# Optimization experiments

Hardware: AMD Instinct MI355X
Metric: run time of the kernel (lower is better)

Reference implementation:

```python
import jax, jax.numpy as jnp
from jax import lax
import numpy as np

B, A, C, H, W = 256, 64, 8, 15, 15
E = 128
CONV_CH = [8, 16, 32, 16, 32]   # in -> hidden[16,32,16] -> out(32)
FLAT = 32 * 7 * 7               # four 3x3 VALID convs: 15 -> 7
MLP_DIMS = [FLAT, 128, 128, 128]


def setup_inputs() -> dict:
    key = jax.random.key(0)
    ks = jax.random.split(key, 16)
    inp = {}
    inp["states"] = jax.random.normal(ks[0], (B, A, C, H, W), jnp.float32)
    # nonnegative weighted adjacency (dense graph, diagonal included like the
    # original loop which always appends (i,i) with weight adj[b,i,i])
    inp["adjacencies"] = jax.random.uniform(ks[1], (B, A, A), jnp.float32)
    for l, (ci, co) in enumerate(zip(CONV_CH[:-1], CONV_CH[1:])):
        inp[f"cw{l}"] = jax.random.normal(ks[2 + l], (co, ci, 3, 3), jnp.float32) * 0.05
        inp[f"cb{l}"] = jnp.zeros((co,), jnp.float32)
    for l, (di, do) in enumerate(zip(MLP_DIMS[:-1], MLP_DIMS[1:])):
        inp[f"mw{l}"] = jax.random.normal(ks[8 + l], (di, do), jnp.float32) * 0.02
        inp[f"mb{l}"] = jnp.zeros((do,), jnp.float32)
    inp["gw"] = jax.random.normal(ks[12], (E, E), jnp.float32) * 0.05
    inp["gb"] = jnp.zeros((E,), jnp.float32)
    return inp


def _conv(x, w, b):
    y = lax.conv_general_dilated(x, w, (1, 1), "VALID",
                                 dimension_numbers=("NCHW", "OIHW", "NCHW"))
    return jax.nn.relu(y + b[None, :, None, None])


def reference(states, adjacencies, cw0, cb0, cw1, cb1, cw2, cb2, cw3, cb3,
              mw0, mb0, mw1, mb1, mw2, mb2, gw, gb):
    b, a, c, h, w = states.shape
    x = states.reshape(b * a, c, h, w)
    # CNN encoder (batched over all B*A agent observations at once)
    for cw, cb in ((cw0, cb0), (cw1, cb1), (cw2, cb2), (cw3, cb3)):
        x = _conv(x, cw, cb)
    x = x.reshape(b * a, -1)
    # MLP: relu on hidden layers, linear output
    x = jax.nn.relu(x @ mw0 + mb0)
    x = jax.nn.relu(x @ mw1 + mb1)
    feats = x @ mw2 + mb2                      # [B*A, E]
    feats = feats.reshape(b, a, E)
    # GCNConv(add_self_loops=False): out = D^{-1/2} A D^{-1/2} aggregation
    # edge (i,j): row=source i, col=target j; deg from target (column sums)
    xw = jnp.einsum("bae,ef->baf", feats, gw)  # x @ W
    deg = adjacencies.sum(axis=1)              # deg[b,j] = sum_i A[b,i,j]
    dinv = jnp.where(deg > 0, 1.0 / jnp.sqrt(jnp.where(deg > 0, deg, 1.0)), 0.0)
    norm = dinv[:, :, None] * adjacencies * dinv[:, None, :]  # N[b,i,j]
    out = jnp.einsum("bij,bie->bje", norm, xw) + gb            # out[b,j] = sum_i N_ij xW_i
    return out.reshape(b * a, E)
```

## Files before the change

### kernel.cpp

```cpp
#include <hip/hip_runtime.h>


typedef short short8 __attribute__((ext_vector_type(8)));
typedef float f32x4  __attribute__((ext_vector_type(4)));

__device__ __forceinline__ unsigned short f2bf(float f) {
    unsigned u = __builtin_bit_cast(unsigned, f);
    u = (u + 0x7FFFu + ((u >> 16) & 1u)) >> 16;
    return (unsigned short)u;
}
__device__ __forceinline__ float bf2f(unsigned short h) {
    unsigned u = ((unsigned)h) << 16;
    return __builtin_bit_cast(float, u);
}

#define ZED_OFF 26304
#define ARENA_FLOATS 6592

__global__ __launch_bounds__(256) void wprep(
    const float* __restrict__ cw0, const float* __restrict__ cw1,
    const float* __restrict__ cw2, const float* __restrict__ cw3,
    short* __restrict__ wbuf)
{
    int gidx = blockIdx.x * 256 + threadIdx.x;
    if (gidx >= 36864) return;
    const float* cw; int base, CI, NM, KIND;
    if (gidx < 3072)       { cw = cw0; base = 0;     CI = 8;  NM = 1; KIND = 0; }
    else if (gidx < 15360) { cw = cw1; base = 3072;  CI = 16; NM = 2; KIND = 1; }
    else if (gidx < 24576) { cw = cw2; base = 15360; CI = 32; NM = 1; KIND = 2; }
    else                   { cw = cw3; base = 24576; CI = 16; NM = 2; KIND = 1; }
    int e = gidx - base;
    int j = e & 7, lane = (e >> 3) & 63, rest = e >> 9;
    int comp = rest & 1, cm = rest >> 1;
    int m = cm % NM, c = cm / NM;
    int g = lane >> 4, colr = lane & 15;
    int co = m * 16 + colr;
    int ky, kx, ci; bool pad = false;
    if (KIND == 0)      { ky = c; kx = g; ci = j; pad = (g >= 3); }
    else if (KIND == 1) {
        ky = c >> 1; int half = c & 1;
        if (half == 0) { kx = g >> 1; ci = (g & 1) * 8 + j; }
        else           { kx = 2;      ci = (g & 1) * 8 + j; pad = (g >= 2); }
    } else              { ky = c / 3; kx = c % 3; ci = g * 8 + j; }
    float w = pad ? 0.0f : cw[((co * CI + ci) * 3 + ky) * 3 + kx];
    unsigned short h = f2bf(w);
    wbuf[gidx] = (comp == 0) ? (short)h : (short)f2bf(w - bf2f(h));
}

__global__ __launch_bounds__(256) void wprep_mlp(
    const float* __restrict__ mw0, const float* __restrict__ mw1,
    const float* __restrict__ mw2, const float* __restrict__ gw,
    short* __restrict__ wp)
{
    int gidx = blockIdx.x * 256 + threadIdx.x;
    if (gidx >= 499712) return;
    const float* W; int base;
    if (gidx < 401408)      { W = mw0; base = 0; }
    else if (gidx < 434176) { W = mw1; base = 401408; }
    else if (gidx < 466944) { W = mw2; base = 434176; }
    else                    { W = gw;  base = 466944; }
    int e = gidx - base;
    int j = e & 7, lane = (e >> 3) & 63, rest = e >> 9;
    int comp = rest & 1, knn = rest >> 1;
    int nn = knn & 7, kc = knn >> 3;
    int k = kc * 32 + (lane >> 4) * 8 + j;
    int n = nn * 16 + (lane & 15);
    float w = W[(size_t)k * 128 + n];
    unsigned short h = f2bf(w);
    wp[gidx] = (comp == 0) ? (short)h : (short)f2bf(w - bf2f(h));
}

template<int CI, int CO, int WIN, int WOUT, int POUT, int NM, int NT,
         int KIND, int INOFF, int NPIN, int OUTOFF, int GOUT>
__device__ __forceinline__ void mfma_layer(
    float* __restrict__ A, const short* __restrict__ wbuf,
    const float* __restrict__ bias, short* __restrict__ gH,
    short* __restrict__ gL, int tid)
{
    const char* Ac = (const char*)A;
    char* Aw = (char*)A;
    const int wv = tid >> 6, lane = tid & 63;
    const int g = lane >> 4, col = lane & 15;
    constexpr int UNITS = NT * NM;
    constexpr int CPK = (KIND == 0) ? 1 : (KIND == 1) ? 2 : 3;
    constexpr int DIN = (CI / 8) * NPIN * 16;
    constexpr int DOUT = (CO / 8) * POUT * 16;
    const int u0 = (UNITS * wv) >> 2, u1 = (UNITS * (wv + 1)) >> 2;

#pragma unroll 1
    for (int u = u0; u < u1; ++u) {
        const int n = u / NM, m = u - n * NM;
        const int p = n * 16 + col;
        const bool valid = (p < POUT);
        const int pix = valid ? p : (POUT - 1);
        const int y = pix / WOUT;
        const int x = pix - y * WOUT;

        f32x4 acc;
        {
            const float4 bv = *(const float4*)(bias + m * 16 + g * 4);
            acc[0] = bv.x; acc[1] = bv.y; acc[2] = bv.z; acc[3] = bv.w;
        }

#pragma unroll
        for (int ky = 0; ky < 3; ++ky) {
#pragma unroll
            for (int cc = 0; cc < CPK; ++cc) {
                int kg, kx; bool okv;
                if (KIND == 0)      { kx = g;      kg = 0;     okv = (g < 3); }
                else if (KIND == 1) {
                    if (cc == 0)    { kx = g >> 1; kg = g & 1; okv = true; }
                    else            { kx = 2;      kg = g & 1; okv = (g < 2); }
                } else              { kx = cc;     kg = g;     okv = true; }
                const int pin = (y + ky) * WIN + x + kx;
                const int vH = okv ? (INOFF + (kg * NPIN + pin) * 16) : ZED_OFF;
                const int vL = okv ? (vH + DIN) : ZED_OFF;
                const int c = ky * CPK + cc;

                const short8 Ah = *(const short8*)(
                    wbuf + ((c * NM + m) * 2 + 0) * 512 + lane * 8);
                const short8 Al = *(const short8*)(
                    wbuf + ((c * NM + m) * 2 + 1) * 512 + lane * 8);

                const short8 Bh = *(const short8*)(Ac + vH);
                acc = __builtin_amdgcn_mfma_f32_16x16x32_bf16(Ah, Bh, acc, 0, 0, 0);
                acc = __builtin_amdgcn_mfma_f32_16x16x32_bf16(Al, Bh, acc, 0, 0, 0);
                const short8 Bl = *(const short8*)(Ac + vL);
                acc = __builtin_amdgcn_mfma_f32_16x16x32_bf16(Ah, Bl, acc, 0, 0, 0);
            }
        }

        if (GOUT) {
            if (valid) {
                const int co0 = m * 16 + g * 4;
#pragma unroll
                for (int r = 0; r < 4; ++r) {
                    float v = fmaxf(acc[r], 0.0f);
                    unsigned short h = f2bf(v);
                    gH[(co0 + r) * POUT + pix] = (short)h;
                    gL[(co0 + r) * POUT + pix] = (short)f2bf(v - bf2f(h));
                }
            }
        } else if (valid) {
            unsigned hh[2], ll[2];
#pragma unroll
            for (int r2 = 0; r2 < 2; ++r2) {
                float v0 = fmaxf(acc[r2 * 2 + 0], 0.0f);
                float v1 = fmaxf(acc[r2 * 2 + 1], 0.0f);
                unsigned short h0 = f2bf(v0), h1 = f2bf(v1);
                unsigned short l0 = f2bf(v0 - bf2f(h0));
                unsigned short l1 = f2bf(v1 - bf2f(h1));
                hh[r2] = (unsigned)h0 | ((unsigned)h1 << 16);
                ll[r2] = (unsigned)l0 | ((unsigned)l1 << 16);
            }
            const int kgO = m * 2 + (g >> 1);
            const int ob2 = OUTOFF + (kgO * POUT + pix) * 16 + (g & 1) * 8;
            *(uint2*)(Aw + ob2)        = make_uint2(hh[0], hh[1]);
            *(uint2*)(Aw + ob2 + DOUT) = make_uint2(ll[0], ll[1]);
        }
    }
}

__global__ __launch_bounds__(256) void conv_mfma(
    const float* __restrict__ states, const short* __restrict__ wbuf,
    const float* __restrict__ cb0, const float* __restrict__ cb1,
    const float* __restrict__ cb2, const float* __restrict__ cb3,
    short* __restrict__ x0h, short* __restrict__ x0l)
{
    __shared__ float A[ARENA_FLOATS];
    const int tid = threadIdx.x;

    if (tid < 4) A[ZED_OFF / 4 + tid] = 0.0f;

    const float* gin = states + (size_t)blockIdx.x * 1800;
    {
        char* Aw = (char*)A;
#pragma unroll
        for (int it = 0; it < 8; ++it) {
            int e = tid + it * 256;
            if (e < 1800) {
                float f = gin[e];
                int ci = e / 225, p = e - ci * 225;
                unsigned short h = f2bf(f);
                unsigned short l = f2bf(f - bf2f(h));
                int off = 10816 + p * 16 + ci * 2;
                *(short*)(Aw + off) = (short)h;
                *(short*)(Aw + off + 3600) = (short)l;
            }
        }
    }
    __syncthreads();

    mfma_layer<8, 16, 15, 13, 169, 1, 11, 0, 10816, 225, 0, 0>(
        A, wbuf + 0, cb0, nullptr, nullptr, tid);
    __syncthreads();
    mfma_layer<16, 32, 13, 11, 121, 2, 8, 1, 0, 169, 10816, 0>(
        A, wbuf + 3072, cb1, nullptr, nullptr, tid);
    __syncthreads();
    mfma_layer<32, 16, 11, 9, 81, 1, 6, 2, 10816, 121, 0, 0>(
        A, wbuf + 15360, cb2, nullptr, nullptr, tid);
    __syncthreads();
    mfma_layer<16, 32, 9, 7, 49, 2, 4, 1, 0, 81, 0, 1>(
        A, wbuf + 24576, cb3,
        x0h + (size_t)blockIdx.x * 1568, x0l + (size_t)blockIdx.x * 1568, tid);
}

template<int KCH, bool RELU, bool OUTF32>
__global__ __launch_bounds__(256) void mgemm(
    const short* __restrict__ Ah, const short* __restrict__ Al,
    const short* __restrict__ wp, const float* __restrict__ bias,
    short* __restrict__ Ch, short* __restrict__ Cl, float* __restrict__ Cf)
{
    constexpr int K = KCH * 32;
    const int tid = threadIdx.x;
    const int wv = tid >> 6, lane = tid & 63;
    const int col = lane & 15, g = lane >> 4;
    const int row0 = blockIdx.x * 64 + wv * 16;
    const size_t aoff = (size_t)(row0 + col) * K + g * 8;

    f32x4 acc[8];
#pragma unroll
    for (int nn = 0; nn < 8; ++nn) {
        float b = bias ? bias[nn * 16 + col] : 0.0f;
        acc[nn][0] = b; acc[nn][1] = b; acc[nn][2] = b; acc[nn][3] = b;
    }

#pragma unroll 2
    for (int kc = 0; kc < KCH; ++kc) {
        const short8 fAh = *(const short8*)(Ah + aoff + kc * 32);
        const short8 fAl = *(const short8*)(Al + aoff + kc * 32);
        const short* wk = wp + (size_t)kc * 8192 + lane * 8;
#pragma unroll
        for (int nn = 0; nn < 8; ++nn) {
            const short8 Bh = *(const short8*)(wk + (nn * 2 + 0) * 512);
            const short8 Bl = *(const short8*)(wk + (nn * 2 + 1) * 512);
            acc[nn] = __builtin_amdgcn_mfma_f32_16x16x32_bf16(fAh, Bh, acc[nn], 0, 0, 0);
            acc[nn] = __builtin_amdgcn_mfma_f32_16x16x32_bf16(fAl, Bh, acc[nn], 0, 0, 0);
            acc[nn] = __builtin_amdgcn_mfma_f32_16x16x32_bf16(fAh, Bl, acc[nn], 0, 0, 0);
        }
    }

#pragma unroll
    for (int nn = 0; nn < 8; ++nn) {
#pragma unroll
        for (int r = 0; r < 4; ++r) {
            float v = acc[nn][r];
            if (RELU) v = fmaxf(v, 0.0f);
            const size_t idx = (size_t)(row0 + g * 4 + r) * 128 + nn * 16 + col;
            if (OUTF32) {
                Cf[idx] = v;
            } else {
                unsigned short h = f2bf(v);
                Ch[idx] = (short)h;
                Cl[idx] = (short)f2bf(v - bf2f(h));
            }
        }
    }
}

__global__ __launch_bounds__(256) void gcn_agg(
    const float* __restrict__ adj, const float* __restrict__ xw,
    const float* __restrict__ gb, float* __restrict__ outp)
{
    __shared__ float sAdj[64 * 64];
    __shared__ float sXW[64 * 128];
    __shared__ float sDinv[64];

    const int b = blockIdx.x;
    const int tid = threadIdx.x;

    const float* ga = adj + (size_t)b * 4096;
#pragma unroll
    for (int it = 0; it < 4; it++) {
        int idx = tid + it * 256;
        *(float4*)(sAdj + idx * 4) = *(const float4*)(ga + idx * 4);
    }
    const float* gx = xw + (size_t)b * 8192;
#pragma unroll
    for (int it = 0; it < 8; it++) {
        int idx = tid + it * 256;
        *(float4*)(sXW + idx * 4) = *(const float4*)(gx + idx * 4);
    }
    __syncthreads();

    if (tid < 64) {
        float d = 0.0f;
        for (int i = 0; i < 64; i++) d += sAdj[i * 64 + tid];
        sDinv[tid] = (d > 0.0f) ? rsqrtf(d) : 0.0f;
    }
    __syncthreads();

#pragma unroll
    for (int it = 0; it < 8; it++) {
        int idx = tid + it * 256;
        int i = idx >> 5;
        float s = sDinv[i];
        float4 v = *(float4*)(sXW + idx * 4);
        v.x *= s; v.y *= s; v.z *= s; v.w *= s;
        *(float4*)(sXW + idx * 4) = v;
    }
    __syncthreads();

    const int j  = tid >> 2;
    const int eb = (tid & 3) * 32;
    float acc[32];
#pragma unroll
    for (int e = 0; e < 32; e++) acc[e] = 0.0f;

    for (int i = 0; i < 64; i++) {
        float wgt = sAdj[i * 64 + j];
        const float* xp = sXW + i * 128 + eb;
#pragma unroll
        for (int e4 = 0; e4 < 8; e4++) {
            float4 v = *(const float4*)(xp + e4 * 4);
            acc[e4 * 4 + 0] += wgt * v.x;
            acc[e4 * 4 + 1] += wgt * v.y;
            acc[e4 * 4 + 2] += wgt * v.z;
            acc[e4 * 4 + 3] += wgt * v.w;
        }
    }

    const float dj = sDinv[j];
    float* go = outp + ((size_t)b * 64 + j) * 128 + eb;
#pragma unroll
    for (int e4 = 0; e4 < 8; e4++) {
        float4 v;
        v.x = acc[e4 * 4 + 0] * dj + gb[eb + e4 * 4 + 0];
        v.y = acc[e4 * 4 + 1] * dj + gb[eb + e4 * 4 + 1];
        v.z = acc[e4 * 4 + 2] * dj + gb[eb + e4 * 4 + 2];
        v.w = acc[e4 * 4 + 3] * dj + gb[eb + e4 * 4 + 3];
        *(float4*)(go + e4 * 4) = v;
    }
}

extern "C" void kernel_launch(void* const* d_in, const int* in_sizes, int n_in,
                              void* d_out, int out_size, void* d_ws, size_t ws_size,
                              hipStream_t stream)
{
    const float* states = (const float*)d_in[0];
    const float* adj    = (const float*)d_in[1];
    const float* cw0 = (const float*)d_in[2];  const float* cb0 = (const float*)d_in[3];
    const float* cw1 = (const float*)d_in[4];  const float* cb1 = (const float*)d_in[5];
    const float* cw2 = (const float*)d_in[6];  const float* cb2 = (const float*)d_in[7];
    const float* cw3 = (const float*)d_in[8];  const float* cb3 = (const float*)d_in[9];
    const float* mw0 = (const float*)d_in[10]; const float* mb0 = (const float*)d_in[11];
    const float* mw1 = (const float*)d_in[12]; const float* mb1 = (const float*)d_in[13];
    const float* mw2 = (const float*)d_in[14]; const float* mb2 = (const float*)d_in[15];
    const float* gw  = (const float*)d_in[16]; const float* gb  = (const float*)d_in[17];

    float* ws = (float*)d_ws;
    const size_t X0E = (size_t)16384 * 1568;

    short* X0h = (short*)ws;
    short* X0l = X0h + X0E;
    short* H1h = (short*)(ws + X0E);
    short* H1l = H1h + 2097152;
    short* H2h = (short*)(ws + X0E + 2097152);
    short* H2l = H2h + 2097152;
    short* WBc = (short*)(ws + X0E + 2 * 2097152);
    short* WPm = WBc + 36864;
    short* Fh = (short*)ws;
    short* Fl = Fh + 2097152;
    float* xw = ws + 2097152;

    float* out = (float*)d_out;

    wprep<<<144, 256, 0, stream>>>(cw0, cw1, cw2, cw3, WBc);
    wprep_mlp<<<1952, 256, 0, stream>>>(mw0, mw1, mw2, gw, WPm);
    conv_mfma<<<16384, 256, 0, stream>>>(states, WBc, cb0, cb1, cb2, cb3,
                                         X0h, X0l);
    mgemm<49, true,  false><<<256, 256, 0, stream>>>(X0h, X0l, WPm + 0,
                                                     mb0, H1h, H1l, nullptr);
    mgemm<4,  true,  false><<<256, 256, 0, stream>>>(H1h, H1l, WPm + 401408,
                                                     mb1, H2h, H2l, nullptr);
    mgemm<4,  false, false><<<256, 256, 0, stream>>>(H2h, H2l, WPm + 434176,
                                                     mb2, Fh, Fl, nullptr);
    mgemm<4,  false, true ><<<256, 256, 0, stream>>>(Fh, Fl, WPm + 466944,
                                                     nullptr, nullptr, nullptr, xw);
    gcn_agg<<<256, 256, 0, stream>>>(adj, xw, gb, out);
}
```

Before: 676.2 us.

## Fuse MLP layers and GCN aggregation into one kernel, merge weight prep kernels

Replaces the four separate MLP/GCN-weight GEMM kernels and the GCN aggregation kernel with a single per-batch kernel that keeps intermediate activations in shared memory as split bf16 hi/lo pairs. The first layer stages X0 tiles through LDS in 128-wide K chunks. The two weight-prep kernels are merged into one launch. This removes global round-trips for the hidden activations and several launch overheads, at the cost of a large LDS footprint per block and extra barriers in the long first-layer K loop.

After: 563.6 us. -16.7%, faster.

```diff
diff --git a/kernel.cpp b/kernel.cpp
--- a/kernel.cpp
+++ b/kernel.cpp
@@ -17,57 +17,54 @@
 #define ZED_OFF 26304
 #define ARENA_FLOATS 6592
 
-__global__ __launch_bounds__(256) void wprep(
+__global__ __launch_bounds__(256) void wprep_all(
     const float* __restrict__ cw0, const float* __restrict__ cw1,
     const float* __restrict__ cw2, const float* __restrict__ cw3,
-    short* __restrict__ wbuf)
+    const float* __restrict__ mw0, const float* __restrict__ mw1,
+    const float* __restrict__ mw2, const float* __restrict__ gw,
+    short* __restrict__ wbuf, short* __restrict__ wp)
 {
     int gidx = blockIdx.x * 256 + threadIdx.x;
-    if (gidx >= 36864) return;
-    const float* cw; int base, CI, NM, KIND;
-    if (gidx < 3072)       { cw = cw0; base = 0;     CI = 8;  NM = 1; KIND = 0; }
-    else if (gidx < 15360) { cw = cw1; base = 3072;  CI = 16; NM = 2; KIND = 1; }
-    else if (gidx < 24576) { cw = cw2; base = 15360; CI = 32; NM = 1; KIND = 2; }
-    else                   { cw = cw3; base = 24576; CI = 16; NM = 2; KIND = 1; }
-    int e = gidx - base;
-    int j = e & 7, lane = (e >> 3) & 63, rest = e >> 9;
-    int comp = rest & 1, cm = rest >> 1;
-    int m = cm % NM, c = cm / NM;
-    int g = lane >> 4, colr = lane & 15;
-    int co = m * 16 + colr;
-    int ky, kx, ci; bool pad = false;
-    if (KIND == 0)      { ky = c; kx = g; ci = j; pad = (g >= 3); }
-    else if (KIND == 1) {
-        ky = c >> 1; int half = c & 1;
-        if (half == 0) { kx = g >> 1; ci = (g & 1) * 8 + j; }
-        else           { kx = 2;      ci = (g & 1) * 8 + j; pad = (g >= 2); }
-    } else              { ky = c / 3; kx = c % 3; ci = g * 8 + j; }
-    float w = pad ? 0.0f : cw[((co * CI + ci) * 3 + ky) * 3 + kx];
-    unsigned short h = f2bf(w);
-    wbuf[gidx] = (comp == 0) ? (short)h : (short)f2bf(w - bf2f(h));
-}
-
-__global__ __launch_bounds__(256) void wprep_mlp(
-    const float* __restrict__ mw0, const float* __restrict__ mw1,
-    const float* __restrict__ mw2, const float* __restrict__ gw,
-    short* __restrict__ wp)
-{
-    int gidx = blockIdx.x * 256 + threadIdx.x;
-    if (gidx >= 499712) return;
-    const float* W; int base;
-    if (gidx < 401408)      { W = mw0; base = 0; }
-    else if (gidx < 434176) { W = mw1; base = 401408; }
-    else if (gidx < 466944) { W = mw2; base = 434176; }
-    else                    { W = gw;  base = 466944; }
-    int e = gidx - base;
-    int j = e & 7, lane = (e >> 3) & 63, rest = e >> 9;
-    int comp = rest & 1, knn = rest >> 1;
-    int nn = knn & 7, kc = knn >> 3;
-    int k = kc * 32 + (lane >> 4) * 8 + j;
-    int n = nn * 16 + (lane & 15);
-    float w = W[(size_t)k * 128 + n];
-    unsigned short h = f2bf(w);
-    wp[gidx] = (comp == 0) ? (short)h : (short)f2bf(w - bf2f(h));
+    if (gidx < 36864) {
+        const float* cw; int base, CI, NM, KIND;
+        if (gidx < 3072)       { cw = cw0; base = 0;     CI = 8;  NM = 1; KIND = 0; }
+        else if (gidx < 15360) { cw = cw1; base = 3072;  CI = 16; NM = 2; KIND = 1; }
+        else if (gidx < 24576) { cw = cw2; base = 15360; CI = 32; NM = 1; KIND = 2; }
+        else                   { cw = cw3; base = 24576; CI = 16; NM = 2; KIND = 1; }
+        int e = gidx - base;
+        int j = e & 7, lane = (e >> 3) & 63, rest = e >> 9;
+        int comp = rest & 1, cm = rest >> 1;
+        int m = cm % NM, c = cm / NM;
+        int g = lane >> 4, colr = lane & 15;
+        int co = m * 16 + colr;
+        int ky, kx, ci; bool pad = false;
+        if (KIND == 0)      { ky = c; kx = g; ci = j; pad = (g >= 3); }
+        else if (KIND == 1) {
+            ky = c >> 1; int half = c & 1;
+            if (half == 0) { kx = g >> 1; ci = (g & 1) * 8 + j; }
+            else           { kx = 2;      ci = (g & 1) * 8 + j; pad = (g >= 2); }
+        } else              { ky = c / 3; kx = c % 3; ci = g * 8 + j; }
+        float w = pad ? 0.0f : cw[((co * CI + ci) * 3 + ky) * 3 + kx];
+        unsigned short h = f2bf(w);
+        wbuf[gidx] = (comp == 0) ? (short)h : (short)f2bf(w - bf2f(h));
+    } else {
+        int e0 = gidx - 36864;
+        if (e0 >= 499712) return;
+        const float* W; int base;
+        if (e0 < 401408)      { W = mw0; base = 0; }
+        else if (e0 < 434176) { W = mw1; base = 401408; }
+        else if (e0 < 466944) { W = mw2; base = 434176; }
+        else                  { W = gw;  base = 466944; }
+        int e = e0 - base;
+        int j = e & 7, lane = (e >> 3) & 63, rest = e >> 9;
+        int comp = rest & 1, knn = rest >> 1;
+        int nn = knn & 7, kc = knn >> 3;
+        int k = kc * 32 + (lane >> 4) * 8 + j;
+        int n = nn * 16 + (lane & 15);
+        float w = W[(size_t)k * 128 + n];
+        unsigned short h = f2bf(w);
+        wp[e0] = (comp == 0) ? (short)h : (short)f2bf(w - bf2f(h));
+    }
 }
 
 template<int CI, int CO, int WIN, int WOUT, int POUT, int NM, int NT,
@@ -205,31 +202,82 @@
         x0h + (size_t)blockIdx.x * 1568, x0l + (size_t)blockIdx.x * 1568, tid);
 }
 
-template<int KCH, bool RELU, bool OUTF32>
-__global__ __launch_bounds__(256) void mgemm(
-    const short* __restrict__ Ah, const short* __restrict__ Al,
-    const short* __restrict__ wp, const float* __restrict__ bias,
-    short* __restrict__ Ch, short* __restrict__ Cl, float* __restrict__ Cf)
+__global__ __launch_bounds__(256) void mlp_gcn(
+    const short* __restrict__ X0h, const short* __restrict__ X0l,
+    const short* __restrict__ wp,
+    const float* __restrict__ mb0, const float* __restrict__ mb1,
+    const float* __restrict__ mb2, const float* __restrict__ adj,
+    const float* __restrict__ gb, float* __restrict__ outp)
 {
-    constexpr int K = KCH * 32;
+    __shared__ short SAh[64 * 132], SAl[64 * 132];
+    __shared__ short SBh[64 * 132], SBl[64 * 132];
+    __shared__ float sXW[64 * 128];
+    __shared__ float sAdj[64 * 64];
+    __shared__ float sDinv[64];
+
+    const int b = blockIdx.x;
     const int tid = threadIdx.x;
     const int wv = tid >> 6, lane = tid & 63;
     const int col = lane & 15, g = lane >> 4;
-    const int row0 = blockIdx.x * 64 + wv * 16;
-    const size_t aoff = (size_t)(row0 + col) * K + g * 8;
+    const int wr0 = wv * 16;
+    const size_t grow = (size_t)b * 64;
+
+    {
+        const float* ga = adj + (size_t)b * 4096;
+#pragma unroll
+        for (int it = 0; it < 4; ++it) {
+            int idx = tid + it * 256;
+            *(float4*)(sAdj + idx * 4) = *(const float4*)(ga + idx * 4);
+        }
+    }
 
     f32x4 acc[8];
 #pragma unroll
     for (int nn = 0; nn < 8; ++nn) {
-        float b = bias ? bias[nn * 16 + col] : 0.0f;
-        acc[nn][0] = b; acc[nn][1] = b; acc[nn][2] = b; acc[nn][3] = b;
-    }
-
-#pragma unroll 2
-    for (int kc = 0; kc < KCH; ++kc) {
-        const short8 fAh = *(const short8*)(Ah + aoff + kc * 32);
-        const short8 fAl = *(const short8*)(Al + aoff + kc * 32);
-        const short* wk = wp + (size_t)kc * 8192 + lane * 8;
+        float bv = mb0[nn * 16 + col];
+        acc[nn][0] = bv; acc[nn][1] = bv; acc[nn][2] = bv; acc[nn][3] = bv;
+    }
+
+#pragma unroll 1
+    for (int ss = 0; ss < 12; ++ss) {
+        const int kbase = ss * 128;
+        __syncthreads();
+#pragma unroll
+        for (int it = 0; it < 4; ++it) {
+            int v = tid + it * 256;
+            int row = v >> 4, u = v & 15;
+            size_t gofs = (grow + row) * 1568 + kbase + u * 8;
+            *(short8*)(SAh + row * 132 + u * 8) = *(const short8*)(X0h + gofs);
+            *(short8*)(SAl + row * 132 + u * 8) = *(const short8*)(X0l + gofs);
+        }
+        __syncthreads();
+#pragma unroll
+        for (int kc = 0; kc < 4; ++kc) {
+            const short8 fAh = *(const short8*)(SAh + (wr0 + col) * 132 + kc * 32 + g * 8);
+            const short8 fAl = *(const short8*)(SAl + (wr0 + col) * 132 + kc * 32 + g * 8);
+            const short* wk = wp + (size_t)(ss * 4 + kc) * 8192 + lane * 8;
+#pragma unroll
+            for (int nn = 0; nn < 8; ++nn) {
+                const short8 Bh = *(const short8*)(wk + (nn * 2 + 0) * 512);
+                const short8 Bl = *(const short8*)(wk + (nn * 2 + 1) * 512);
+                acc[nn] = __builtin_amdgcn_mfma_f32_16x16x32_bf16(fAh, Bh, acc[nn], 0, 0, 0);
+                acc[nn] = __builtin_amdgcn_mfma_f32_16x16x32_bf16(fAl, Bh, acc[nn], 0, 0, 0);
+                acc[nn] = __builtin_amdgcn_mfma_f32_16x16x32_bf16(fAh, Bl, acc[nn], 0, 0, 0);
+            }
+        }
+    }
+    __syncthreads();
+    {
+        int row = tid >> 2, u = tid & 3;
+        size_t gofs = (grow + row) * 1568 + 1536 + u * 8;
+        *(short8*)(SAh + row * 132 + u * 8) = *(const short8*)(X0h + gofs);
+        *(short8*)(SAl + row * 132 + u * 8) = *(const short8*)(X0l + gofs);
+    }
+    __syncthreads();
+    {
+        const short8 fAh = *(const short8*)(SAh + (wr0 + col) * 132 + g * 8);
+        const short8 fAl = *(const short8*)(SAl + (wr0 + col) * 132 + g * 8);
+        const short* wk = wp + (size_t)48 * 8192 + lane * 8;
 #pragma unroll
         for (int nn = 0; nn < 8; ++nn) {
             const short8 Bh = *(const short8*)(wk + (nn * 2 + 0) * 512);
@@ -239,48 +287,104 @@
             acc[nn] = __builtin_amdgcn_mfma_f32_16x16x32_bf16(fAh, Bl, acc[nn], 0, 0, 0);
         }
     }
+    __syncthreads();
+#pragma unroll
+    for (int nn = 0; nn < 8; ++nn)
+#pragma unroll
+        for (int r = 0; r < 4; ++r) {
+            float v = fmaxf(acc[nn][r], 0.0f);
+            unsigned short h = f2bf(v);
+            int row = wr0 + g * 4 + r;
+            SBh[row * 132 + nn * 16 + col] = (short)h;
+            SBl[row * 132 + nn * 16 + col] = (short)f2bf(v - bf2f(h));
+        }
+    __syncthreads();
 
 #pragma unroll
     for (int nn = 0; nn < 8; ++nn) {
+        float bv = mb1[nn * 16 + col];
+        acc[nn][0] = bv; acc[nn][1] = bv; acc[nn][2] = bv; acc[nn][3] = bv;
+    }
+#pragma unroll
+    for (int kc = 0; kc < 4; ++kc) {
+        const short8 fAh = *(const short8*)(SBh + (wr0 + col) * 132 + kc * 32 + g * 8);
+        const short8 fAl = *(const short8*)(SBl + (wr0 + col) * 132 + kc * 32 + g * 8);
+        const short* wk = wp + 401408 + (size_t)kc * 8192 + lane * 8;
+#pragma unroll
+        for (int nn = 0; nn < 8; ++nn) {
+            const short8 Bh = *(const short8*)(wk + (nn * 2 + 0) * 512);
+            const short8 Bl = *(const short8*)(wk + (nn * 2 + 1) * 512);
+            acc[nn] = __builtin_amdgcn_mfma_f32_16x16x32_bf16(fAh, Bh, acc[nn], 0, 0, 0);
+            acc[nn] = __builtin_amdgcn_mfma_f32_16x16x32_bf16(fAl, Bh, acc[nn], 0, 0, 0);
+            acc[nn] = __builtin_amdgcn_mfma_f32_16x16x32_bf16(fAh, Bl, acc[nn], 0, 0, 0);
+        }
+    }
+#pragma unroll
+    for (int nn = 0; nn < 8; ++nn)
+#pragma unroll
+        for (int r = 0; r < 4; ++r) {
+            float v = fmaxf(acc[nn][r], 0.0f);
+            unsigned short h = f2bf(v);
+            int row = wr0 + g * 4 + r;
+            SAh[row * 132 + nn * 16 + col] = (short)h;
+            SAl[row * 132 + nn * 16 + col] = (short)f2bf(v - bf2f(h));
+        }
+    __syncthreads();
+
+#pragma unroll
+    for (int nn = 0; nn < 8; ++nn) {
+        float bv = mb2[nn * 16 + col];
+        acc[nn][0] = bv; acc[nn][1] = bv; acc[nn][2] = bv; acc[nn][3] = bv;
+    }
+#pragma unroll
+    for (int kc = 0; kc < 4; ++kc) {
+        const short8 fAh = *(const short8*)(SAh + (wr0 + col) * 132 + kc * 32 + g * 8);
+        const short8 fAl = *(const short8*)(SAl + (wr0 + col) * 132 + kc * 32 + g * 8);
+        const short* wk = wp + 434176 + (size_t)kc * 8192 + lane * 8;
+#pragma unroll
+        for (int nn = 0; nn < 8; ++nn) {
+            const short8 Bh = *(const short8*)(wk + (nn * 2 + 0) * 512);
+            const short8 Bl = *(const short8*)(wk + (nn * 2 + 1) * 512);
+            acc[nn] = __builtin_amdgcn_mfma_f32_16x16x32_bf16(fAh, Bh, acc[nn], 0, 0, 0);
+            acc[nn] = __builtin_amdgcn_mfma_f32_16x16x32_bf16(fAl, Bh, acc[nn], 0, 0, 0);
+            acc[nn] = __builtin_amdgcn_mfma_f32_16x16x32_bf16(fAh, Bl, acc[nn], 0, 0, 0);
+        }
+    }
+#pragma unroll
+    for (int nn = 0; nn < 8; ++nn)
 #pragma unroll
         for (int r = 0; r < 4; ++r) {
             float v = acc[nn][r];
-            if (RELU) v = fmaxf(v, 0.0f);
-            const size_t idx = (size_t)(row0 + g * 4 + r) * 128 + nn * 16 + col;
-            if (OUTF32) {
-                Cf[idx] = v;
-            } else {
-                unsigned short h = f2bf(v);
-                Ch[idx] = (short)h;
-                Cl[idx] = (short)f2bf(v - bf2f(h));
-            }
-        }
-    }
-}
-
-__global__ __launch_bounds__(256) void gcn_agg(
-    const float* __restrict__ adj, const float* __restrict__ xw,
-    const float* __restrict__ gb, float* __restrict__ outp)
-{
-    __shared__ float sAdj[64 * 64];
-    __shared__ float sXW[64 * 128];
-    __shared__ float sDinv[64];
-
-    const int b = blockIdx.x;
-    const int tid = threadIdx.x;
-
-    const float* ga = adj + (size_t)b * 4096;
-#pragma unroll
-    for (int it = 0; it < 4; it++) {
-        int idx = tid + it * 256;
-        *(float4*)(sAdj + idx * 4) = *(const float4*)(ga + idx * 4);
-    }
-    const float* gx = xw + (size_t)b * 8192;
-#pragma unroll
-    for (int it = 0; it < 8; it++) {
-        int idx = tid + it * 256;
-        *(float4*)(sXW + idx * 4) = *(const float4*)(gx + idx * 4);
-    }
+            unsigned short h = f2bf(v);
+            int row = wr0 + g * 4 + r;
+            SBh[row * 132 + nn * 16 + col] = (short)h;
+            SBl[row * 132 + nn * 16 + col] = (short)f2bf(v - bf2f(h));
+        }
+    __syncthreads();
+
+#pragma unroll
+    for (int nn = 0; nn < 8; ++nn) {
+        acc[nn][0] = 0.0f; acc[nn][1] = 0.0f; acc[nn][2] = 0.0f; acc[nn][3] = 0.0f;
+    }
+#pragma unroll
+    for (int kc = 0; kc < 4; ++kc) {
+        const short8 fAh = *(const short8*)(SBh + (wr0 + col) * 132 + kc * 32 + g * 8);
+        const short8 fAl = *(const short8*)(SBl + (wr0 + col) * 132 + kc * 32 + g * 8);
+        const short* wk = wp + 466944 + (size_t)kc * 8192 + lane * 8;
+#pragma unroll
+        for (int nn = 0; nn < 8; ++nn) {
+            const short8 Bh = *(const short8*)(wk + (nn * 2 + 0) * 512);
+            const short8 Bl = *(const short8*)(wk + (nn * 2 + 1) * 512);
+            acc[nn] = __builtin_amdgcn_mfma_f32_16x16x32_bf16(fAh, Bh, acc[nn], 0, 0, 0);
+            acc[nn] = __builtin_amdgcn_mfma_f32_16x16x32_bf16(fAl, Bh, acc[nn], 0, 0, 0);
+            acc[nn] = __builtin_amdgcn_mfma_f32_16x16x32_bf16(fAh, Bl, acc[nn], 0, 0, 0);
+        }
+    }
+#pragma unroll
+    for (int nn = 0; nn < 8; ++nn)
+#pragma unroll
+        for (int r = 0; r < 4; ++r)
+            sXW[(wr0 + g * 4 + r) * 128 + nn * 16 + col] = acc[nn][r];
     __syncthreads();
 
     if (tid < 64) {
@@ -303,9 +407,9 @@
 
     const int j  = tid >> 2;
     const int eb = (tid & 3) * 32;
-    float acc[32];
-#pragma unroll
-    for (int e = 0; e < 32; e++) acc[e] = 0.0f;
+    float ac[32];
+#pragma unroll
+    for (int e = 0; e < 32; e++) ac[e] = 0.0f;
 
     for (int i = 0; i < 64; i++) {
         float wgt = sAdj[i * 64 + j];
@@ -313,10 +417,10 @@
 #pragma unroll
         for (int e4 = 0; e4 < 8; e4++) {
             float4 v = *(const float4*)(xp + e4 * 4);
-            acc[e4 * 4 + 0] += wgt * v.x;
-            acc[e4 * 4 + 1] += wgt * v.y;
-            acc[e4 * 4 + 2] += wgt * v.z;
-            acc[e4 * 4 + 3] += wgt * v.w;
+            ac[e4 * 4 + 0] += wgt * v.x;
+            ac[e4 * 4 + 1] += wgt * v.y;
+            ac[e4 * 4 + 2] += wgt * v.z;
+            ac[e4 * 4 + 3] += wgt * v.w;
         }
     }
 
@@ -325,10 +429,10 @@
 #pragma unroll
     for (int e4 = 0; e4 < 8; e4++) {
         float4 v;
-        v.x = acc[e4 * 4 + 0] * dj + gb[eb + e4 * 4 + 0];
-        v.y = acc[e4 * 4 + 1] * dj + gb[eb + e4 * 4 + 1];
-        v.z = acc[e4 * 4 + 2] * dj + gb[eb + e4 * 4 + 2];
-        v.w = acc[e4 * 4 + 3] * dj + gb[eb + e4 * 4 + 3];
+        v.x = ac[e4 * 4 + 0] * dj + gb[eb + e4 * 4 + 0];
+        v.y = ac[e4 * 4 + 1] * dj + gb[eb + e4 * 4 + 1];
+        v.z = ac[e4 * 4 + 2] * dj + gb[eb + e4 * 4 + 2];
+        v.w = ac[e4 * 4 + 3] * dj + gb[eb + e4 * 4 + 3];
         *(float4*)(go + e4 * 4) = v;
     }
 }
@@ -348,34 +452,18 @@
     const float* mw2 = (const float*)d_in[14]; const float* mb2 = (const float*)d_in[15];
     const float* gw  = (const float*)d_in[16]; const float* gb  = (const float*)d_in[17];
 
-    float* ws = (float*)d_ws;
     const size_t X0E = (size_t)16384 * 1568;
-
-    short* X0h = (short*)ws;
+    short* X0h = (short*)d_ws;
     short* X0l = X0h + X0E;
-    short* H1h = (short*)(ws + X0E);
-    short* H1l = H1h + 2097152;
-    short* H2h = (short*)(ws + X0E + 2097152);
-    short* H2l = H2h + 2097152;
-    short* WBc = (short*)(ws + X0E + 2 * 2097152);
+    short* WBc = X0l + X0E;
     short* WPm = WBc + 36864;
-    short* Fh = (short*)ws;
-    short* Fl = Fh + 2097152;
-    float* xw = ws + 2097152;
 
     float* out = (float*)d_out;
 
-    wprep<<<144, 256, 0, stream>>>(cw0, cw1, cw2, cw3, WBc);
-    wprep_mlp<<<1952, 256, 0, stream>>>(mw0, mw1, mw2, gw, WPm);
+    wprep_all<<<2096, 256, 0, stream>>>(cw0, cw1, cw2, cw3,
+                                        mw0, mw1, mw2, gw, WBc, WPm);
     conv_mfma<<<16384, 256, 0, stream>>>(states, WBc, cb0, cb1, cb2, cb3,
                                          X0h, X0l);
-    mgemm<49, true,  false><<<256, 256, 0, stream>>>(X0h, X0l, WPm + 0,
-                                                     mb0, H1h, H1l, nullptr);
-    mgemm<4,  true,  false><<<256, 256, 0, stream>>>(H1h, H1l, WPm + 401408,
-                                                     mb1, H2h, H2l, nullptr);
-    mgemm<4,  false, false><<<256, 256, 0, stream>>>(H2h, H2l, WPm + 434176,
-                                                     mb2, Fh, Fl, nullptr);
-    mgemm<4,  false, true ><<<256, 256, 0, stream>>>(Fh, Fl, WPm + 466944,
-                                                     nullptr, nullptr, nullptr, xw);
-    gcn_agg<<<256, 256, 0, stream>>>(adj, xw, gb, out);
-}
+    mlp_gcn<<<256, 256, 0, stream>>>(X0h, X0l, WPm, mb0, mb1, mb2,
+                                     adj, gb, out);
+}
```
